# Kernel tuning notes

Measured on AMD Instinct MI355X. Metric: run time of the kernel, lower is better.

## Reference

```python
import jax, jax.numpy as jnp
import numpy as np

B, T, DIN, D = 8, 2048, 512, 1024
LN_EPS = 1e-5


def setup_inputs() -> dict:
    key = jax.random.key(0)
    k0, k1, k2, k3 = jax.random.split(key, 4)
    x = jax.random.normal(k0, (B, T, DIN), jnp.float32)
    # Linear params (torch layout: W [out, in]); delta_proj bias is zero-init per module
    Wd = jax.random.normal(k1, (D, DIN), jnp.float32) / np.sqrt(DIN)
    bd = jnp.zeros((D,), jnp.float32)
    Wb = jax.random.normal(k2, (D, DIN), jnp.float32) / np.sqrt(DIN)
    bb = jax.random.normal(k3, (D,), jnp.float32) * 0.01
    A_log = jnp.log(jnp.linspace(1.0, 16.0, D, dtype=jnp.float32))
    threshold = jnp.ones((D,), jnp.float32)
    gamma = jnp.ones((D,), jnp.float32)
    beta = jnp.zeros((D,), jnp.float32)
    h0 = jnp.zeros((B, D), jnp.float32)
    return {"x": x, "Wd": Wd, "bd": bd, "Wb": Wb, "bb": bb,
            "A_log": A_log, "threshold": threshold,
            "gamma": gamma, "beta": beta, "h0": h0}


def reference(x, Wd, bd, Wb, bb, A_log, threshold, gamma, beta, h0):
    # Input-dependent step parameters (computed once, outside the scan)
    delta = jax.nn.softplus(jnp.einsum('btc,dc->btd', x, Wd) + bd)   # [B,T,D]
    b_step = delta * (jnp.einsum('btc,dc->btd', x, Wb) + bb)          # [B,T,D]
    A_step = jnp.exp(-delta * jnp.exp(A_log))                         # [B,T,D]

    def step(h, ab):
        a, b = ab                      # each [B,D]
        h = a * h + b
        s = (h - threshold > 0).astype(x.dtype)   # spike (non-differentiable)
        h = h * (1.0 - s)                          # hard reset
        return h, (h, s)

    # scan over time: move T to the leading axis
    _, (h_post, spikes) = jax.lax.scan(
        step, h0, (A_step.transpose(1, 0, 2), b_step.transpose(1, 0, 2)))
    h_post = h_post.transpose(1, 0, 2)   # [B,T,D]
    spikes = spikes.transpose(1, 0, 2)   # [B,T,D]

    # LayerNorm over last dim
    mu = jnp.mean(h_post, axis=-1, keepdims=True)
    var = jnp.mean(jnp.square(h_post - mu), axis=-1, keepdims=True)
    out = (h_post - mu) * jax.lax.rsqrt(var + LN_EPS) * gamma + beta
    return (out, spikes)
```

## Files before the change

### kernel.cpp

```cpp
#include <hip/hip_runtime.h>
#include <cmath>

constexpr int Bb  = 8;
constexpr int Tt  = 2048;
constexpr int DIN = 512;
constexpr int Dd  = 1024;
constexpr long long BT  = (long long)Bb * Tt;
constexpr long long BTD = BT * Dd;

__device__ __forceinline__ float np_expf(float x) {
  const float LOG2E = 1.4426950408889634074f;
  const float MAGIC = 12582912.0f;
  const float C1 = -6.93145752e-1f;
  const float C2 = -1.42860677e-6f;
  const float P0 = 9.999999999980870924916e-01f;
  const float P1 = 7.257664613233124478488e-01f;
  const float P2 = 2.473615434895520810817e-01f;
  const float P3 = 5.114512081637298353406e-02f;
  const float P4 = 6.757896990527504603057e-03f;
  const float P5 = 5.082762527590693718096e-04f;
  const float Q0 = 1.0f;
  const float Q1 = -2.742335390411667452936e-01f;
  const float Q2 = 2.159509375685829852307e-02f;
  const float XMAX = 88.72283935546875f;
  const float XMIN = -87.3365478515625f;
  if (!(x == x)) return x;
  if (x > XMAX)  return __builtin_inff();
  if (x < XMIN)  return 0.0f;
  float q = __fsub_rn(fmaf(x, LOG2E, MAGIC), MAGIC);
  float r = fmaf(q, C1, x);
  r = fmaf(q, C2, r);
  float num = fmaf(r, P5, P4);
  num = fmaf(num, r, P3);
  num = fmaf(num, r, P2);
  num = fmaf(num, r, P1);
  num = fmaf(num, r, P0);
  float den = fmaf(r, Q2, Q1);
  den = fmaf(den, r, Q0);
  float p = __fdiv_rn(num, den);
  return ldexpf(p, (int)q);
}

__device__ __forceinline__ float expf_cr(float x) { return (float)exp((double)x); }

__device__ __forceinline__ float log1pf_fd(float x) {
  const float ln2_hi = __int_as_float(0x3f317180);
  const float ln2_lo = __int_as_float(0x3717f7d1);
  const float Lp1 = __int_as_float(0x3F2AAAAB), Lp2 = __int_as_float(0x3ECCCCCD),
              Lp3 = __int_as_float(0x3E924925), Lp4 = __int_as_float(0x3E638E29),
              Lp5 = __int_as_float(0x3E3A3325), Lp6 = __int_as_float(0x3E1CD04F),
              Lp7 = __int_as_float(0x3E178897);
  int hx = __float_as_int(x);
  int ax = hx & 0x7fffffff;
  int k = 1, hu = 0;
  float f = 0.f, c = 0.f, u;
  if (hx < 0x3ed413d7) {
    if (ax < 0x38000000) {
      if (ax < 0x33800000) return x;
      return __fsub_rn(x, __fmul_rn(__fmul_rn(x, x), 0.5f));
    }
    if (hx > 0 || hx <= (int)0xbe95f61f) { k = 0; f = x; hu = 1; }
  }
  if (k != 0) {
    if (hx < 0x4b800000) {
      u = __fadd_rn(1.0f, x);
      int hu0 = __float_as_int(u);
      k = (hu0 >> 23) - 127;
      c = (k > 0) ? __fsub_rn(1.0f, __fsub_rn(u, x))
                  : __fsub_rn(x, __fsub_rn(u, 1.0f));
      c = __fdiv_rn(c, u);
      hu = hu0;
    } else {
      u = x; hu = __float_as_int(u); k = (hu >> 23) - 127; c = 0.f;
    }
    hu &= 0x007fffff;
    if (hu < 0x3504f7) { u = __int_as_float(hu | 0x3f800000); }
    else { k += 1; u = __int_as_float(hu | 0x3f000000); hu = (0x00800000 - hu) >> 2; }
    f = __fsub_rn(u, 1.0f);
  }
  float hfsq = __fmul_rn(__fmul_rn(0.5f, f), f);
  if (hu == 0) {
    if (f == 0.0f) {
      if (k == 0) return 0.0f;
      c = __fadd_rn(c, __fmul_rn((float)k, ln2_lo));
      return __fadd_rn(__fmul_rn((float)k, ln2_hi), c);
    }
    float R = __fmul_rn(hfsq, __fsub_rn(1.0f, __fmul_rn(0.66666668653f, f)));
    if (k == 0) return __fsub_rn(f, R);
    return __fsub_rn(__fmul_rn((float)k, ln2_hi),
           __fsub_rn(__fsub_rn(R, __fadd_rn(__fmul_rn((float)k, ln2_lo), c)), f));
  }
  float s = __fdiv_rn(f, __fadd_rn(2.0f, f));
  float z = __fmul_rn(s, s);
  float pz = __fadd_rn(Lp6, __fmul_rn(z, Lp7));
  pz = __fadd_rn(Lp5, __fmul_rn(z, pz));
  pz = __fadd_rn(Lp4, __fmul_rn(z, pz));
  pz = __fadd_rn(Lp3, __fmul_rn(z, pz));
  pz = __fadd_rn(Lp2, __fmul_rn(z, pz));
  pz = __fadd_rn(Lp1, __fmul_rn(z, pz));
  float R = __fmul_rn(z, pz);
  if (k == 0)
    return __fsub_rn(f, __fsub_rn(hfsq, __fmul_rn(s, __fadd_rn(hfsq, R))));
  return __fsub_rn(__fmul_rn((float)k, ln2_hi),
         __fsub_rn(__fsub_rn(hfsq, __fadd_rn(__fmul_rn(s, __fadd_rn(hfsq, R)),
                   __fadd_rn(__fmul_rn((float)k, ln2_lo), c))), f));
}

__device__ __forceinline__ float np_softplus(float x) {
  if (x == 0.0f) return __int_as_float(0x3F317218);
  if (x > 0.0f)  return __fadd_rn(x, log1pf_fd(expf_cr(-x)));
  return log1pf_fd(expf_cr(x));
}

#define BM 128
#define BN 128
#define BK 32

__global__ __launch_bounds__(256, 2) void gemm_np(
    const float* __restrict__ x,  const float* __restrict__ Wd,
    const float* __restrict__ bd, const float* __restrict__ Wb,
    const float* __restrict__ bb, const float* __restrict__ A_log,
    float* __restrict__ Aarr, float* __restrict__ Barr)
{
  __shared__ float xsT[BK][BM];
  __shared__ float wds[BK][BN];
  __shared__ float wbs[BK][BN];

  const int tid = threadIdx.x;
  const int bn0 = blockIdx.x * BN;
  const int bm0 = blockIdx.y * BM;
  const int tx  = tid & 15;
  const int mg  = tid >> 4;

  const int wn    = tid & 127;
  const int whalf = tid >> 7;

  float accd[8][8], accb[8][8];
#pragma unroll
  for (int i = 0; i < 8; ++i)
#pragma unroll
    for (int j = 0; j < 8; ++j) { accd[i][j] = 0.f; accb[i][j] = 0.f; }

  for (int kt = 0; kt < DIN / BK; ++kt) {
    const int k0 = kt * BK;
    __syncthreads();
#pragma unroll
    for (int p = 0; p < 4; ++p) {
      int f = p * 256 + tid;
      int m = f >> 3;
      int q = f & 7;
      float4 v = *(const float4*)&x[(size_t)(bm0 + m) * DIN + k0 + q * 4];
      int col = m ^ (q << 3);
      xsT[q*4+0][col] = v.x;
      xsT[q*4+1][col] = v.y;
      xsT[q*4+2][col] = v.z;
      xsT[q*4+3][col] = v.w;
    }
#pragma unroll
    for (int p = 0; p < 4; ++p) {
      int kq = whalf * 4 + p;
      const size_t g = (size_t)(bn0 + wn) * DIN + k0 + kq * 4;
      float4 vd = *(const float4*)&Wd[g];
      float4 vb = *(const float4*)&Wb[g];
      int col = (((wn >> 2) ^ kq) << 2) | (wn & 3);
      wds[kq*4+0][col] = vd.x; wds[kq*4+1][col] = vd.y;
      wds[kq*4+2][col] = vd.z; wds[kq*4+3][col] = vd.w;
      wbs[kq*4+0][col] = vb.x; wbs[kq*4+1][col] = vb.y;
      wbs[kq*4+2][col] = vb.z; wbs[kq*4+3][col] = vb.w;
    }
    __syncthreads();

#pragma unroll 2
    for (int kq = 0; kq < BK / 4; ++kq) {
      const int xc0 = (mg * 8)     ^ (kq << 3);
      const int xc1 = (mg * 8 + 4) ^ (kq << 3);
      const int wc0 = ((tx * 2)     ^ kq) << 2;
      const int wc1 = ((tx * 2 + 1) ^ kq) << 2;
#pragma unroll
      for (int t = 0; t < 4; ++t) {
        const int k = kq * 4 + t;
        float4 x0 = *(const float4*)&xsT[k][xc0];
        float4 x1 = *(const float4*)&xsT[k][xc1];
        float4 d0 = *(const float4*)&wds[k][wc0];
        float4 d1 = *(const float4*)&wds[k][wc1];
        float4 b0 = *(const float4*)&wbs[k][wc0];
        float4 b1 = *(const float4*)&wbs[k][wc1];
        float xa[8]  = {x0.x, x0.y, x0.z, x0.w, x1.x, x1.y, x1.z, x1.w};
        float wd8[8] = {d0.x, d0.y, d0.z, d0.w, d1.x, d1.y, d1.z, d1.w};
        float wb8[8] = {b0.x, b0.y, b0.z, b0.w, b1.x, b1.y, b1.z, b1.w};
#pragma unroll
        for (int i = 0; i < 8; ++i) {
          const float xv = xa[i];
#pragma unroll
          for (int j = 0; j < 8; ++j) {
            accd[i][j] = __fadd_rn(accd[i][j], __fmul_rn(xv, wd8[j]));
            accb[i][j] = __fadd_rn(accb[i][j], __fmul_rn(xv, wb8[j]));
          }
        }
      }
    }
  }

  const int n0 = bn0 + tx * 8;
  float bd8[8], bb8[8], eA8[8];
#pragma unroll
  for (int j = 0; j < 8; ++j) {
    bd8[j] = bd[n0 + j];
    bb8[j] = bb[n0 + j];
    eA8[j] = np_expf(A_log[n0 + j]);
  }
#pragma unroll
  for (int i = 0; i < 8; ++i) {
    const int m = bm0 + mg * 8 + i;
    float av[8], bv[8];
#pragma unroll
    for (int j = 0; j < 8; ++j) {
      float z1b = __fadd_rn(accd[i][j], bd8[j]);
      float z2b = __fadd_rn(accb[i][j], bb8[j]);
      float delta = np_softplus(z1b);
      float w  = __fmul_rn(delta, eA8[j]);
      av[j] = np_expf(-w);
      bv[j] = __fmul_rn(delta, z2b);
    }
    float* Ap = &Aarr[(size_t)m * Dd + n0];
    float* Bp = &Barr[(size_t)m * Dd + n0];
    *(float4*)(Ap)     = make_float4(av[0], av[1], av[2], av[3]);
    *(float4*)(Ap + 4) = make_float4(av[4], av[5], av[6], av[7]);
    *(float4*)(Bp)     = make_float4(bv[0], bv[1], bv[2], bv[3]);
    *(float4*)(Bp + 4) = make_float4(bv[4], bv[5], bv[6], bv[7]);
  }
}

__global__ __launch_bounds__(64) void scan_np(
    const float* __restrict__ thr_arr, const float* __restrict__ h0,
    float* __restrict__ Aarr, float* __restrict__ Barr)
{
  const int bx = blockIdx.x;
  const int b  = bx >> 4;
  const int d  = ((bx & 15) << 6) + threadIdx.x;

  const float thr = thr_arr[d];
  float h = h0[(size_t)b * Dd + d];

  float* Ap = Aarr + (size_t)b * Tt * Dd + d;
  float* Bp = Barr + (size_t)b * Tt * Dd + d;

  constexpr int PF = 32;
  float pa[PF], pb[PF];
#pragma unroll
  for (int k = 0; k < PF; ++k) {
    pa[k] = Ap[(size_t)k * Dd];
    pb[k] = Bp[(size_t)k * Dd];
  }

  for (int t0 = 0; t0 < Tt; t0 += PF) {
    const int t1 = t0 + PF;
    float na[PF], nb[PF];
    if (t1 < Tt) {
#pragma unroll
      for (int k = 0; k < PF; ++k) {
        na[k] = Ap[(size_t)(t1 + k) * Dd];
        nb[k] = Bp[(size_t)(t1 + k) * Dd];
      }
    }
#pragma unroll
    for (int k = 0; k < PF; ++k) {
      h = __fadd_rn(__fmul_rn(pa[k], h), pb[k]);
      const bool spike = __fsub_rn(h, thr) > 0.0f;
      h = spike ? 0.0f : h;
      Ap[(size_t)(t0 + k) * Dd] = h;
      Bp[(size_t)(t0 + k) * Dd] = spike ? 1.0f : 0.0f;
    }
    if (t1 < Tt) {
#pragma unroll
      for (int k = 0; k < PF; ++k) { pa[k] = na[k]; pb[k] = nb[k]; }
    }
  }
}

__global__ __launch_bounds__(256) void ln_np(
    const float* __restrict__ gamma, const float* __restrict__ beta,
    float* __restrict__ H)
{
  const int row = blockIdx.x;
  const int tid = threadIdx.x;
  const size_t base = (size_t)row * Dd + (tid << 2);

  float4 v = *(const float4*)&H[base];

  __shared__ double red[4];
  __shared__ double red2[4];
  const int wave = tid >> 6, lane = tid & 63;

  double sum = (double)v.x + (double)v.y + (double)v.z + (double)v.w;
#pragma unroll
  for (int off = 32; off > 0; off >>= 1) sum += __shfl_down(sum, off);
  if (lane == 0) red[wave] = sum;
  __syncthreads();
  const float muf = (float)((red[0] + red[1] + red[2] + red[3]) * (1.0 / Dd));

  float dx0 = __fsub_rn(v.x, muf), dx1 = __fsub_rn(v.y, muf);
  float dx2 = __fsub_rn(v.z, muf), dx3 = __fsub_rn(v.w, muf);
  double sq = (double)dx0*dx0 + (double)dx1*dx1 + (double)dx2*dx2 + (double)dx3*dx3;
#pragma unroll
  for (int off = 32; off > 0; off >>= 1) sq += __shfl_down(sq, off);
  if (lane == 0) red2[wave] = sq;
  __syncthreads();
  const float varf = (float)((red2[0] + red2[1] + red2[2] + red2[3]) * (1.0 / Dd));
  const float invf = __fdiv_rn(1.0f, __fsqrt_rn(__fadd_rn(varf, 1e-5f)));

  const int n = tid << 2;
  float4 g  = *(const float4*)&gamma[n];
  float4 be = *(const float4*)&beta[n];
  float4 o;
  o.x = __fadd_rn(__fmul_rn(__fmul_rn(dx0, invf), g.x), be.x);
  o.y = __fadd_rn(__fmul_rn(__fmul_rn(dx1, invf), g.y), be.y);
  o.z = __fadd_rn(__fmul_rn(__fmul_rn(dx2, invf), g.z), be.z);
  o.w = __fadd_rn(__fmul_rn(__fmul_rn(dx3, invf), g.w), be.w);
  *(float4*)&H[base] = o;
}

extern "C" void kernel_launch(void* const* d_in, const int* in_sizes, int n_in,
                              void* d_out, int out_size, void* d_ws, size_t ws_size,
                              hipStream_t stream)
{
  const float* x     = (const float*)d_in[0];
  const float* Wd    = (const float*)d_in[1];
  const float* bd    = (const float*)d_in[2];
  const float* Wb    = (const float*)d_in[3];
  const float* bb    = (const float*)d_in[4];
  const float* A_log = (const float*)d_in[5];
  const float* thr   = (const float*)d_in[6];
  const float* gamma = (const float*)d_in[7];
  const float* beta  = (const float*)d_in[8];
  const float* h0    = (const float*)d_in[9];

  float* out  = (float*)d_out;
  float* Aarr = out;
  float* Barr = out + (size_t)BTD;

  dim3 g1(Dd / BN, (int)(BT / BM));
  gemm_np<<<g1, 256, 0, stream>>>(x, Wd, bd, Wb, bb, A_log, Aarr, Barr);
  scan_np<<<128, 64, 0, stream>>>(thr, h0, Aarr, Barr);
  ln_np<<<(int)BT, 256, 0, stream>>>(gamma, beta, Aarr);
}
```

Before: 696.9 us.

## Prefetch GEMM tiles into registers before barrier and remap thread-to-column layout

Global loads for x, Wd and Wb tiles are issued into registers before the first barrier of each k-step, so memory latency can overlap the wait on the previous compute. The thread mapping for W loads and the column assignment per thread change: each thread now owns two 4-wide column groups 64 apart, with a new XOR swizzle. This is meant to reduce LDS bank conflicts and make epilogue stores coalesce better. The occupancy hint of 2 blocks per CU is dropped, so the compiler may use more registers and lower occupancy.

```diff
diff --git a/kernel.cpp b/kernel.cpp
--- a/kernel.cpp
+++ b/kernel.cpp
@@ -116,7 +116,7 @@
 #define BN 128
 #define BK 32
 
-__global__ __launch_bounds__(256, 2) void gemm_np(
+__global__ __launch_bounds__(256) void gemm_np(
     const float* __restrict__ x,  const float* __restrict__ Wd,
     const float* __restrict__ bd, const float* __restrict__ Wb,
     const float* __restrict__ bb, const float* __restrict__ A_log,
@@ -132,8 +132,8 @@
   const int tx  = tid & 15;
   const int mg  = tid >> 4;
 
-  const int wn    = tid & 127;
-  const int whalf = tid >> 7;
+  const int sr8 = tid >> 3;
+  const int sq  = tid & 7;
 
   float accd[8][8], accb[8][8];
 #pragma unroll
@@ -143,48 +143,68 @@
 
   for (int kt = 0; kt < DIN / BK; ++kt) {
     const int k0 = kt * BK;
+    float4 lx0 = *(const float4*)&x[(size_t)(bm0 +  0 + sr8) * DIN + k0 + sq * 4];
+    float4 lx1 = *(const float4*)&x[(size_t)(bm0 + 32 + sr8) * DIN + k0 + sq * 4];
+    float4 lx2 = *(const float4*)&x[(size_t)(bm0 + 64 + sr8) * DIN + k0 + sq * 4];
+    float4 lx3 = *(const float4*)&x[(size_t)(bm0 + 96 + sr8) * DIN + k0 + sq * 4];
+    float4 ld0 = *(const float4*)&Wd[(size_t)(bn0 +  0 + sr8) * DIN + k0 + sq * 4];
+    float4 ld1 = *(const float4*)&Wd[(size_t)(bn0 + 32 + sr8) * DIN + k0 + sq * 4];
+    float4 ld2 = *(const float4*)&Wd[(size_t)(bn0 + 64 + sr8) * DIN + k0 + sq * 4];
+    float4 ld3 = *(const float4*)&Wd[(size_t)(bn0 + 96 + sr8) * DIN + k0 + sq * 4];
+    float4 lb0 = *(const float4*)&Wb[(size_t)(bn0 +  0 + sr8) * DIN + k0 + sq * 4];
+    float4 lb1 = *(const float4*)&Wb[(size_t)(bn0 + 32 + sr8) * DIN + k0 + sq * 4];
+    float4 lb2 = *(const float4*)&Wb[(size_t)(bn0 + 64 + sr8) * DIN + k0 + sq * 4];
+    float4 lb3 = *(const float4*)&Wb[(size_t)(bn0 + 96 + sr8) * DIN + k0 + sq * 4];
     __syncthreads();
-#pragma unroll
-    for (int p = 0; p < 4; ++p) {
-      int f = p * 256 + tid;
-      int m = f >> 3;
-      int q = f & 7;
-      float4 v = *(const float4*)&x[(size_t)(bm0 + m) * DIN + k0 + q * 4];
-      int col = m ^ (q << 3);
-      xsT[q*4+0][col] = v.x;
-      xsT[q*4+1][col] = v.y;
-      xsT[q*4+2][col] = v.z;
-      xsT[q*4+3][col] = v.w;
-    }
-#pragma unroll
-    for (int p = 0; p < 4; ++p) {
-      int kq = whalf * 4 + p;
-      const size_t g = (size_t)(bn0 + wn) * DIN + k0 + kq * 4;
-      float4 vd = *(const float4*)&Wd[g];
-      float4 vb = *(const float4*)&Wb[g];
-      int col = (((wn >> 2) ^ kq) << 2) | (wn & 3);
-      wds[kq*4+0][col] = vd.x; wds[kq*4+1][col] = vd.y;
-      wds[kq*4+2][col] = vd.z; wds[kq*4+3][col] = vd.w;
-      wbs[kq*4+0][col] = vb.x; wbs[kq*4+1][col] = vb.y;
-      wbs[kq*4+2][col] = vb.z; wbs[kq*4+3][col] = vb.w;
+    {
+      int r0 = sr8, r1 = 32 + sr8, r2 = 64 + sr8, r3 = 96 + sr8;
+      int c0 = r0 ^ (sq << 3), c1 = r1 ^ (sq << 3);
+      int c2 = r2 ^ (sq << 3), c3 = r3 ^ (sq << 3);
+      xsT[sq*4+0][c0] = lx0.x; xsT[sq*4+1][c0] = lx0.y;
+      xsT[sq*4+2][c0] = lx0.z; xsT[sq*4+3][c0] = lx0.w;
+      xsT[sq*4+0][c1] = lx1.x; xsT[sq*4+1][c1] = lx1.y;
+      xsT[sq*4+2][c1] = lx1.z; xsT[sq*4+3][c1] = lx1.w;
+      xsT[sq*4+0][c2] = lx2.x; xsT[sq*4+1][c2] = lx2.y;
+      xsT[sq*4+2][c2] = lx2.z; xsT[sq*4+3][c2] = lx2.w;
+      xsT[sq*4+0][c3] = lx3.x; xsT[sq*4+1][c3] = lx3.y;
+      xsT[sq*4+2][c3] = lx3.z; xsT[sq*4+3][c3] = lx3.w;
+    }
+    {
+      int n0 = sr8, n1 = 32 + sr8, n2 = 64 + sr8, n3 = 96 + sr8;
+      int c0 = n0 ^ (sq << 2), c1 = n1 ^ (sq << 2);
+      int c2 = n2 ^ (sq << 2), c3 = n3 ^ (sq << 2);
+      wds[sq*4+0][c0] = ld0.x; wds[sq*4+1][c0] = ld0.y;
+      wds[sq*4+2][c0] = ld0.z; wds[sq*4+3][c0] = ld0.w;
+      wds[sq*4+0][c1] = ld1.x; wds[sq*4+1][c1] = ld1.y;
+      wds[sq*4+2][c1] = ld1.z; wds[sq*4+3][c1] = ld1.w;
+      wds[sq*4+0][c2] = ld2.x; wds[sq*4+1][c2] = ld2.y;
+      wds[sq*4+2][c2] = ld2.z; wds[sq*4+3][c2] = ld2.w;
+      wds[sq*4+0][c3] = ld3.x; wds[sq*4+1][c3] = ld3.y;
+      wds[sq*4+2][c3] = ld3.z; wds[sq*4+3][c3] = ld3.w;
+      wbs[sq*4+0][c0] = lb0.x; wbs[sq*4+1][c0] = lb0.y;
+      wbs[sq*4+2][c0] = lb0.z; wbs[sq*4+3][c0] = lb0.w;
+      wbs[sq*4+0][c1] = lb1.x; wbs[sq*4+1][c1] = lb1.y;
+      wbs[sq*4+2][c1] = lb1.z; wbs[sq*4+3][c1] = lb1.w;
+      wbs[sq*4+0][c2] = lb2.x; wbs[sq*4+1][c2] = lb2.y;
+      wbs[sq*4+2][c2] = lb2.z; wbs[sq*4+3][c2] = lb2.w;
+      wbs[sq*4+0][c3] = lb3.x; wbs[sq*4+1][c3] = lb3.y;
+      wbs[sq*4+2][c3] = lb3.z; wbs[sq*4+3][c3] = lb3.w;
     }
     __syncthreads();
 
 #pragma unroll 2
     for (int kq = 0; kq < BK / 4; ++kq) {
-      const int xc0 = (mg * 8)     ^ (kq << 3);
-      const int xc1 = (mg * 8 + 4) ^ (kq << 3);
-      const int wc0 = ((tx * 2)     ^ kq) << 2;
-      const int wc1 = ((tx * 2 + 1) ^ kq) << 2;
+      const int xc = (mg * 8) ^ (kq << 3);
+      const int wc = 4 * (tx ^ kq);
 #pragma unroll
       for (int t = 0; t < 4; ++t) {
         const int k = kq * 4 + t;
-        float4 x0 = *(const float4*)&xsT[k][xc0];
-        float4 x1 = *(const float4*)&xsT[k][xc1];
-        float4 d0 = *(const float4*)&wds[k][wc0];
-        float4 d1 = *(const float4*)&wds[k][wc1];
-        float4 b0 = *(const float4*)&wbs[k][wc0];
-        float4 b1 = *(const float4*)&wbs[k][wc1];
+        float4 x0 = *(const float4*)&xsT[k][xc];
+        float4 x1 = *(const float4*)&xsT[k][xc + 4];
+        float4 d0 = *(const float4*)&wds[k][wc];
+        float4 d1 = *(const float4*)&wds[k][wc + 64];
+        float4 b0 = *(const float4*)&wbs[k][wc];
+        float4 b1 = *(const float4*)&wbs[k][wc + 64];
         float xa[8]  = {x0.x, x0.y, x0.z, x0.w, x1.x, x1.y, x1.z, x1.w};
         float wd8[8] = {d0.x, d0.y, d0.z, d0.w, d1.x, d1.y, d1.z, d1.w};
         float wb8[8] = {b0.x, b0.y, b0.z, b0.w, b1.x, b1.y, b1.z, b1.w};
@@ -201,13 +221,15 @@
     }
   }
 
-  const int n0 = bn0 + tx * 8;
+  const int na = bn0 + tx * 4;
+  const int nb = na + 64;
   float bd8[8], bb8[8], eA8[8];
 #pragma unroll
-  for (int j = 0; j < 8; ++j) {
-    bd8[j] = bd[n0 + j];
-    bb8[j] = bb[n0 + j];
-    eA8[j] = np_expf(A_log[n0 + j]);
+  for (int j = 0; j < 4; ++j) {
+    bd8[j]   = bd[na + j];  bd8[4+j] = bd[nb + j];
+    bb8[j]   = bb[na + j];  bb8[4+j] = bb[nb + j];
+    eA8[j]   = np_expf(A_log[na + j]);
+    eA8[4+j] = np_expf(A_log[nb + j]);
   }
 #pragma unroll
   for (int i = 0; i < 8; ++i) {
@@ -222,12 +244,12 @@
       av[j] = np_expf(-w);
       bv[j] = __fmul_rn(delta, z2b);
     }
-    float* Ap = &Aarr[(size_t)m * Dd + n0];
-    float* Bp = &Barr[(size_t)m * Dd + n0];
-    *(float4*)(Ap)     = make_float4(av[0], av[1], av[2], av[3]);
-    *(float4*)(Ap + 4) = make_float4(av[4], av[5], av[6], av[7]);
-    *(float4*)(Bp)     = make_float4(bv[0], bv[1], bv[2], bv[3]);
-    *(float4*)(Bp + 4) = make_float4(bv[4], bv[5], bv[6], bv[7]);
+    float* Ap = &Aarr[(size_t)m * Dd];
+    float* Bp = &Barr[(size_t)m * Dd];
+    *(float4*)(Ap + na) = make_float4(av[0], av[1], av[2], av[3]);
+    *(float4*)(Ap + nb) = make_float4(av[4], av[5], av[6], av[7]);
+    *(float4*)(Bp + na) = make_float4(bv[0], bv[1], bv[2], bv[3]);
+    *(float4*)(Bp + nb) = make_float4(bv[4], bv[5], bv[6], bv[7]);
   }
 }
 
```

New measurement: 665.8 us. 1.05x faster.
